# Kernel optimization log

Hardware: AMD Instinct MI355X
Metric: run time of the kernel (lower is better)

Reference implementation:

```python
import jax, jax.numpy as jnp
import numpy as np

EPS = 1e-5
T = 8          # n_segment
PATCH = 3      # corr_size


def _bn(x, g, b):
    # eval-mode BatchNorm with running_mean=0, running_var=1 (init values)
    shape = (1, -1) + (1,) * (x.ndim - 2)
    inv = 1.0 / jnp.sqrt(1.0 + EPS)
    return x * (g * inv).reshape(shape) + b.reshape(shape)


def setup_inputs() -> dict:
    key = jax.random.key(0)
    k1, k2, k3 = jax.random.split(key, 3)
    nt, c, h, w = 64, 256, 56, 56
    cr = 64  # c // reduction, reduction = 4
    return {
        "x": jax.random.normal(k1, (nt, c, h, w), dtype=jnp.float32),
        "conv21_w": jax.random.normal(k2, (cr, c), dtype=jnp.float32) * 0.05,
        "bn21_g": jnp.ones((cr,), jnp.float32),
        "bn21_b": jnp.zeros((cr,), jnp.float32),
        "bn22_g": jnp.ones((PATCH * PATCH,), jnp.float32),
        "bn22_b": jnp.zeros((PATCH * PATCH,), jnp.float32),
        "conv22_w": jax.random.normal(k3, (c, PATCH * PATCH), dtype=jnp.float32) * 0.05,
        "bn23_g": jnp.ones((c,), jnp.float32),
        "bn23_b": jnp.zeros((c,), jnp.float32),
    }


def reference(x, conv21_w, bn21_g, bn21_b, bn22_g, bn22_b, conv22_w, bn23_g, bn23_b):
    nt, c, h, w = x.shape
    n = nt // T
    cr = conv21_w.shape[0]
    residual = x

    # (n, c, T, h, w)
    xv = x.reshape(n, T, c, h, w).transpose(0, 2, 1, 3, 4)
    # conv21: 1x1x1 Conv3d c -> cr, no bias
    y = jnp.einsum('oc,ncthw->nothw', conv21_w, xv)
    y = jax.nn.relu(_bn(y, bn21_g, bn21_b))

    # temporally shifted copy: frame t paired with frame min(t+1, T-1)
    idx = jnp.minimum(jnp.arange(1, T + 1), T - 1)
    y2 = y[:, :, idx, :, :]

    # flatten back to (nt, cr, h, w)
    x1 = y.transpose(0, 2, 1, 3, 4).reshape(nt, cr, h, w)
    x2 = y2.transpose(0, 2, 1, 3, 4).reshape(nt, cr, h, w)

    # SpatialCorrelationSampler(kernel_size=1, patch_size=3): zero-padded
    # displacements (dy, dx) in {-1,0,1}^2, dot product over channels.
    pad = PATCH // 2
    x2p = jnp.pad(x2, ((0, 0), (0, 0), (pad, pad), (pad, pad)))
    cv = jnp.stack(
        [jnp.einsum('nchw,nchw->nhw', x1, x2p[:, :, dy:dy + h, dx:dx + w])
         for dy in range(PATCH) for dx in range(PATCH)],
        axis=1,
    ) / cr  # (nt, 9, h, w), divided by c // (reduction * corr_group)

    cv = jax.nn.relu(_bn(cv, bn22_g, bn22_b))
    # conv22: 1x1 Conv2d 9 -> c, no bias
    out = jnp.einsum('ok,nkhw->nohw', conv22_w, cv)
    out = _bn(out, bn23_g, bn23_b) + residual
    return jax.nn.relu(out)
```

## Files before the change

kernel.cpp:

```cpp
#include <hip/hip_runtime.h>

#define HW     3136
#define WIDTH  56
#define C      256
#define CR     64
#define NT     64
#define TT     8
#define PW     64
#define PH     58
#define YPLANE (PH*PW)
#define YBYTES ((size_t)NT * CR * YPLANE * 2)
#define CVBYTES ((size_t)NT * 9 * HW * 4)

#define BN_INV 0.9999950000374997f

typedef __attribute__((ext_vector_type(8))) short short8;
typedef __attribute__((ext_vector_type(8))) unsigned short ushort8;
typedef __attribute__((ext_vector_type(4))) float f32x4;
typedef __attribute__((ext_vector_type(2))) float f32x2;

static __device__ __forceinline__ float relu(float v) { return fmaxf(v, 0.0f); }
static __device__ __forceinline__ float bf2f(unsigned short u) {
    return __builtin_bit_cast(float, (unsigned)u << 16);
}
static __device__ __forceinline__ unsigned short f2bf(float f) {
    unsigned u = __builtin_bit_cast(unsigned, f);
    unsigned r = (u + 0x7FFFu + ((u >> 16) & 1u)) >> 16;
    return (unsigned short)r;
}
static __device__ __forceinline__ unsigned pack2(float a, float b) {
    return (unsigned)f2bf(a) | ((unsigned)f2bf(b) << 16);
}

__global__ __launch_bounds__(256) void k0_cvt_w(const float* __restrict__ w,
                                                unsigned short* __restrict__ wbf) {
    int i = blockIdx.x * 256 + threadIdx.x;
    wbf[i] = f2bf(w[i]);
}

static __device__ __forceinline__ void halo_zero(int nt, int tid,
                                                 unsigned short* __restrict__ y) {
    const int ch = tid >> 2, part = tid & 3;
    unsigned short* pl = y + ((size_t)nt * CR + ch) * YPLANE;
    if (part == 0) {
        ushort8 z = (ushort8)0;
#pragma unroll
        for (int j = 0; j < 8; ++j) *(ushort8*)(pl + j * 8) = z;
    } else if (part == 1) {
        ushort8 z = (ushort8)0;
        unsigned short* q = pl + 57 * PW;
#pragma unroll
        for (int j = 0; j < 8; ++j) *(ushort8*)(q + j * 8) = z;
    } else if (part == 2) {
        for (int r = 1; r <= 28; ++r) {
            unsigned short* q = pl + r * PW + 57;
#pragma unroll
            for (int j = 0; j < 8; ++j) q[j] = 0;
        }
    } else {
        for (int r = 29; r <= 56; ++r) {
            unsigned short* q = pl + r * PW + 57;
#pragma unroll
            for (int j = 0; j < 8; ++j) q[j] = 0;
        }
        pl[PW] = 0;
    }
}

template<int TP>
__global__ __launch_bounds__(256) void k1_mfma(const float* __restrict__ x,
                                               const unsigned short* __restrict__ wbf,
                                               const float* __restrict__ g,
                                               const float* __restrict__ bb,
                                               unsigned short* __restrict__ y) {
    constexpr int NB = TP / 64;
    constexpr int NQ = TP / 4;
    __shared__ unsigned short Bl[2][NQ][136];

    const int tid  = threadIdx.x;
    const int lane = tid & 63;
    const int wv   = tid >> 6;

    int nt, px0;
    if (TP == 256) {
        if (blockIdx.x >= 768) { halo_zero(blockIdx.x - 768, tid, y); return; }
        nt = blockIdx.x / 12; px0 = (blockIdx.x % 12) * 256;
    } else {
        nt = blockIdx.x; px0 = 3072;
    }

    const int p4 = tid & (NQ - 1);
    const int c8 = tid / NQ;
    const bool active = (TP == 256) ? true : (c8 < 4);

    const float* xbase = x + (size_t)nt * (C * HW) + px0 + 4 * p4;
    const int frow = lane & 15;
    const int hi   = lane >> 4;
    const unsigned short* abase = wbf + frow * C + hi * 8;

    f32x4 acc[NB][4];
#pragma unroll
    for (int nb = 0; nb < NB; ++nb)
#pragma unroll
        for (int mb = 0; mb < 4; ++mb) acc[nb][mb] = (f32x4)0.0f;

    f32x4  xq[8];
    short8 afr[2][4];

#define LOADB(KS)                                                          \
    if (active) {                                                          \
        const float* _p = xbase + (size_t)((KS) * 32 + c8 * 8) * HW;       \
        _Pragma("unroll")                                                  \
        for (int j = 0; j < 8; ++j) xq[j] = *(const f32x4*)(_p + (size_t)j * HW); \
    }

#define LOADA(KS, DST)                                                     \
    _Pragma("unroll")                                                      \
    for (int mb = 0; mb < 4; ++mb)                                         \
        (DST)[mb] = *(const short8*)(abase + mb * 16 * C + (KS) * 32);

#define WRITEB(BUF)                                                        \
    if (active) {                                                          \
        _Pragma("unroll")                                                  \
        for (int i = 0; i < 4; ++i) {                                      \
            union { unsigned d[4]; short8 v; } pk;                         \
            pk.d[0] = pack2(xq[0][i], xq[1][i]);                           \
            pk.d[1] = pack2(xq[2][i], xq[3][i]);                           \
            pk.d[2] = pack2(xq[4][i], xq[5][i]);                           \
            pk.d[3] = pack2(xq[6][i], xq[7][i]);                           \
            *(short8*)&Bl[BUF][p4][i * 32 + ((c8 ^ i) & 3) * 8] = pk.v;    \
        }                                                                  \
    }

    LOADB(0)
    LOADA(0, afr[0])
    WRITEB(0)
    __syncthreads();

#pragma unroll
    for (int ks = 0; ks < 8; ++ks) {
        const int cb = ks & 1;
        if (ks < 7) {
            LOADB(ks + 1)
            LOADA(ks + 1, afr[cb ^ 1])
        }
        short8 bfrag[NB];
#pragma unroll
        for (int nb = 0; nb < NB; ++nb) {
            const int pxl = wv * (TP / 4) + nb * 16 + frow;
            bfrag[nb] = *(const short8*)
                &Bl[cb][pxl >> 2][(pxl & 3) * 32 + ((hi ^ (pxl & 3)) & 3) * 8];
        }
#pragma unroll
        for (int nb = 0; nb < NB; ++nb)
#pragma unroll
            for (int mb = 0; mb < 4; ++mb)
                acc[nb][mb] = __builtin_amdgcn_mfma_f32_16x16x32_bf16(
                    afr[cb][mb], bfrag[nb], acc[nb][mb], 0, 0, 0);
        if (ks < 7) {
            WRITEB(cb ^ 1)
            __syncthreads();
        }
    }
#undef LOADB
#undef LOADA
#undef WRITEB

    unsigned short* ybase = y + (size_t)nt * CR * YPLANE;
#pragma unroll
    for (int nb = 0; nb < NB; ++nb) {
        const int p = px0 + wv * (TP / 4) + nb * 16 + frow;
        const int r = p / WIDTH;
        const int c = p - r * WIDTH;
        const int pidx = (r + 1) * PW + (c + 1);
#pragma unroll
        for (int mb = 0; mb < 4; ++mb)
#pragma unroll
            for (int rr = 0; rr < 4; ++rr) {
                int o = mb * 16 + hi * 4 + rr;
                float v = relu(fmaf(acc[nb][mb][rr], g[o] * BN_INV, bb[o]));
                ybase[(size_t)o * YPLANE + pidx] = f2bf(v);
            }
    }
}

__global__ __launch_bounds__(256) void k2_corr(const unsigned short* __restrict__ y,
                                               const float* __restrict__ g,
                                               const float* __restrict__ bb,
                                               float* __restrict__ cv) {
    int gt   = blockIdx.x * 256 + threadIdx.x;
    int h    = gt & 3;
    int task = gt >> 2;
    int nt   = task / 392;
    int rm   = task - nt * 392;
    int r    = rm / 7;
    int cg   = rm - r * 7;
    int c0   = cg * 8;
    int nt2  = ((nt & (TT - 1)) < TT - 1) ? nt + 1 : nt;

    const unsigned short* y1 = y + ((size_t)nt * CR + h * 16) * YPLANE
                                 + (size_t)(r + 1) * PW + c0;
    const unsigned short* y2 = y + ((size_t)nt2 * CR + h * 16) * YPLANE
                                 + (size_t)r * PW + c0;

    float acc[9][8];
#pragma unroll
    for (int k = 0; k < 9; ++k)
#pragma unroll
        for (int px = 0; px < 8; ++px) acc[k][px] = 0.0f;

#pragma unroll 2
    for (int ch = 0; ch < 16; ++ch) {
        const unsigned short* p1 = y1 + (size_t)ch * YPLANE;
        ushort8 a8 = *(const ushort8*)p1;
        unsigned at = *(const unsigned*)(p1 + 8);
        float a[8];
#pragma unroll
        for (int j = 0; j < 7; ++j) a[j] = bf2f(a8[j + 1]);
        a[7] = bf2f((unsigned short)(at & 0xffffu));

        const unsigned short* p2 = y2 + (size_t)ch * YPLANE;
#pragma unroll
        for (int dy = 0; dy < 3; ++dy) {
            const unsigned short* pr = p2 + dy * PW;
            ushort8 b8 = *(const ushort8*)pr;
            unsigned bt = *(const unsigned*)(pr + 8);
            float w[10];
#pragma unroll
            for (int j = 0; j < 8; ++j) w[j] = bf2f(b8[j]);
            w[8] = bf2f((unsigned short)(bt & 0xffffu));
            w[9] = bf2f((unsigned short)(bt >> 16));
#pragma unroll
            for (int dx = 0; dx < 3; ++dx) {
                int k = dy * 3 + dx;
#pragma unroll
                for (int px = 0; px < 8; ++px)
                    acc[k][px] = fmaf(a[px], w[px + dx], acc[k][px]);
            }
        }
    }

#pragma unroll
    for (int k = 0; k < 9; ++k)
#pragma unroll
        for (int px = 0; px < 8; ++px) {
            float v = acc[k][px];
            v += __shfl_xor(v, 1);
            v += __shfl_xor(v, 2);
            acc[k][px] = v;
        }

    if (h == 0) {
        float* cp = cv + (size_t)nt * 9 * HW + r * WIDTH + c0;
        const float rcr = 1.0f / CR;
#pragma unroll
        for (int k = 0; k < 9; ++k) {
            float sc = g[k] * BN_INV, bv = bb[k];
            f32x4 lo, hi;
            lo.x = relu(fmaf(acc[k][0] * rcr, sc, bv));
            lo.y = relu(fmaf(acc[k][1] * rcr, sc, bv));
            lo.z = relu(fmaf(acc[k][2] * rcr, sc, bv));
            lo.w = relu(fmaf(acc[k][3] * rcr, sc, bv));
            hi.x = relu(fmaf(acc[k][4] * rcr, sc, bv));
            hi.y = relu(fmaf(acc[k][5] * rcr, sc, bv));
            hi.z = relu(fmaf(acc[k][6] * rcr, sc, bv));
            hi.w = relu(fmaf(acc[k][7] * rcr, sc, bv));
            *(f32x4*)(cp + (size_t)k * HW)     = lo;
            *(f32x4*)(cp + (size_t)k * HW + 4) = hi;
        }
    }
}

__global__ __launch_bounds__(256) void k3_conv22(const float* __restrict__ cv,
                                                 const float* __restrict__ w2,
                                                 const float* __restrict__ g,
                                                 const float* __restrict__ bb,
                                                 const float* __restrict__ x,
                                                 float* __restrict__ out) {
    int gt = blockIdx.x * 256 + threadIdx.x;
    int nt = gt / 1568;
    int p2 = (gt - nt * 1568) * 2;

    const float* cp = cv + (size_t)nt * 9 * HW + p2;
    float cvx[9], cvy[9];
#pragma unroll
    for (int k = 0; k < 9; ++k) {
        f32x2 v = *(const f32x2*)(cp + (size_t)k * HW);
        cvx[k] = v.x; cvy[k] = v.y;
    }

    const float* xp = x   + (size_t)nt * (C * HW) + p2;
    float*       op = out + (size_t)nt * (C * HW) + p2;

#pragma unroll 8
    for (int o = 0; o < C; ++o) {
        const float* wr = w2 + o * 9;
        f32x2 xr = *(const f32x2*)(xp + (size_t)o * HW);
        float sx = 0.0f, sy = 0.0f;
#pragma unroll
        for (int k = 0; k < 9; ++k) {
            float wv = wr[k];
            sx = fmaf(wv, cvx[k], sx);
            sy = fmaf(wv, cvy[k], sy);
        }
        float sc = g[o] * BN_INV, bv = bb[o];
        f32x2 rv;
        rv.x = relu(fmaf(sx, sc, bv) + xr.x);
        rv.y = relu(fmaf(sy, sc, bv) + xr.y);
        *(f32x2*)(op + (size_t)o * HW) = rv;
    }
}

extern "C" void kernel_launch(void* const* d_in, const int* in_sizes, int n_in,
                              void* d_out, int out_size, void* d_ws, size_t ws_size,
                              hipStream_t stream) {
    const float* x   = (const float*)d_in[0];
    const float* w21 = (const float*)d_in[1];
    const float* g21 = (const float*)d_in[2];
    const float* b21 = (const float*)d_in[3];
    const float* g22 = (const float*)d_in[4];
    const float* b22 = (const float*)d_in[5];
    const float* w22 = (const float*)d_in[6];
    const float* g23 = (const float*)d_in[7];
    const float* b23 = (const float*)d_in[8];
    float* out = (float*)d_out;

    unsigned short* yb  = (unsigned short*)d_ws;
    float*          cvb = (float*)((char*)d_ws + YBYTES);
    unsigned short* wbf = (unsigned short*)((char*)d_ws + YBYTES + CVBYTES);

    k0_cvt_w     <<<64,  256, 0, stream>>>(w21, wbf);
    k1_mfma<256> <<<832, 256, 0, stream>>>(x, wbf, g21, b21, yb);
    k1_mfma<64>  <<<64,  256, 0, stream>>>(x, wbf, g21, b21, yb);
    k2_corr      <<<392, 256, 0, stream>>>(yb, g22, b22, cvb);
    k3_conv22    <<<392, 256, 0, stream>>>(cvb, w22, g23, b23, x, out);
}
```

Baseline: 195.7 us.

## Shrink per-thread work across all stages to raise block counts and occupancy

Measured after the change: 202.3 us. 3.3% more time.

```diff
diff --git a/kernel.cpp b/kernel.cpp
--- a/kernel.cpp
+++ b/kernel.cpp
@@ -23,6 +23,12 @@
 static __device__ __forceinline__ float bf2f(unsigned short u) {
     return __builtin_bit_cast(float, (unsigned)u << 16);
 }
+static __device__ __forceinline__ float bfLO(unsigned u) {
+    return __builtin_bit_cast(float, u << 16);
+}
+static __device__ __forceinline__ float bfHI(unsigned u) {
+    return __builtin_bit_cast(float, u & 0xFFFF0000u);
+}
 static __device__ __forceinline__ unsigned short f2bf(float f) {
     unsigned u = __builtin_bit_cast(unsigned, f);
     unsigned r = (u + 0x7FFFu + ((u >> 16) & 1u)) >> 16;
@@ -82,16 +88,16 @@
     const int wv   = tid >> 6;
 
     int nt, px0;
-    if (TP == 256) {
-        if (blockIdx.x >= 768) { halo_zero(blockIdx.x - 768, tid, y); return; }
-        nt = blockIdx.x / 12; px0 = (blockIdx.x % 12) * 256;
+    if (TP == 128) {
+        if (blockIdx.x >= 1536) { halo_zero(blockIdx.x - 1536, tid, y); return; }
+        nt = blockIdx.x / 24; px0 = (blockIdx.x % 24) * 128;
     } else {
         nt = blockIdx.x; px0 = 3072;
     }
 
     const int p4 = tid & (NQ - 1);
     const int c8 = tid / NQ;
-    const bool active = (TP == 256) ? true : (c8 < 4);
+    const bool active = (c8 < 4);
 
     const float* xbase = x + (size_t)nt * (C * HW) + px0 + 4 * p4;
     const int frow = lane & 15;
@@ -105,7 +111,7 @@
         for (int mb = 0; mb < 4; ++mb) acc[nb][mb] = (f32x4)0.0f;
 
     f32x4  xq[8];
-    short8 afr[2][4];
+    short8 afr[4];
 
 #define LOADB(KS)                                                          \
     if (active) {                                                          \
@@ -113,11 +119,6 @@
         _Pragma("unroll")                                                  \
         for (int j = 0; j < 8; ++j) xq[j] = *(const f32x4*)(_p + (size_t)j * HW); \
     }
-
-#define LOADA(KS, DST)                                                     \
-    _Pragma("unroll")                                                      \
-    for (int mb = 0; mb < 4; ++mb)                                         \
-        (DST)[mb] = *(const short8*)(abase + mb * 16 * C + (KS) * 32);
 
 #define WRITEB(BUF)                                                        \
     if (active) {                                                          \
@@ -133,17 +134,16 @@
     }
 
     LOADB(0)
-    LOADA(0, afr[0])
     WRITEB(0)
     __syncthreads();
 
 #pragma unroll
     for (int ks = 0; ks < 8; ++ks) {
         const int cb = ks & 1;
-        if (ks < 7) {
-            LOADB(ks + 1)
-            LOADA(ks + 1, afr[cb ^ 1])
-        }
+        if (ks < 7) { LOADB(ks + 1) }
+#pragma unroll
+        for (int mb = 0; mb < 4; ++mb)
+            afr[mb] = *(const short8*)(abase + mb * 16 * C + ks * 32);
         short8 bfrag[NB];
 #pragma unroll
         for (int nb = 0; nb < NB; ++nb) {
@@ -156,14 +156,13 @@
 #pragma unroll
             for (int mb = 0; mb < 4; ++mb)
                 acc[nb][mb] = __builtin_amdgcn_mfma_f32_16x16x32_bf16(
-                    afr[cb][mb], bfrag[nb], acc[nb][mb], 0, 0, 0);
+                    afr[mb], bfrag[nb], acc[nb][mb], 0, 0, 0);
         if (ks < 7) {
             WRITEB(cb ^ 1)
             __syncthreads();
         }
     }
 #undef LOADB
-#undef LOADA
 #undef WRITEB
 
     unsigned short* ybase = y + (size_t)nt * CR * YPLANE;
@@ -188,53 +187,44 @@
                                                const float* __restrict__ g,
                                                const float* __restrict__ bb,
                                                float* __restrict__ cv) {
-    int gt   = blockIdx.x * 256 + threadIdx.x;
-    int h    = gt & 3;
-    int task = gt >> 2;
-    int nt   = task / 392;
-    int rm   = task - nt * 392;
-    int r    = rm / 7;
-    int cg   = rm - r * 7;
-    int c0   = cg * 8;
-    int nt2  = ((nt & (TT - 1)) < TT - 1) ? nt + 1 : nt;
-
-    const unsigned short* y1 = y + ((size_t)nt * CR + h * 16) * YPLANE
-                                 + (size_t)(r + 1) * PW + c0;
-    const unsigned short* y2 = y + ((size_t)nt2 * CR + h * 16) * YPLANE
-                                 + (size_t)r * PW + c0;
-
-    float acc[9][8];
+    const int gt   = blockIdx.x * 256 + threadIdx.x;
+    const int h    = gt & 7;
+    const int task = gt >> 3;
+    const int nt   = task / 784;
+    const int rm   = task - nt * 784;
+    const int r    = rm / 14;
+    const int cg   = rm - r * 14;
+    const int c0   = cg * 4;
+    const int nt2  = ((nt & (TT - 1)) < TT - 1) ? nt + 1 : nt;
+
+    const unsigned* y1 = (const unsigned*)(y + ((size_t)nt * CR + h * 8) * YPLANE
+                                             + (size_t)(r + 1) * PW + c0);
+    const unsigned* y2 = (const unsigned*)(y + ((size_t)nt2 * CR + h * 8) * YPLANE
+                                             + (size_t)r * PW + c0);
+
+    float acc[9][4];
 #pragma unroll
     for (int k = 0; k < 9; ++k)
 #pragma unroll
-        for (int px = 0; px < 8; ++px) acc[k][px] = 0.0f;
-
-#pragma unroll 2
-    for (int ch = 0; ch < 16; ++ch) {
-        const unsigned short* p1 = y1 + (size_t)ch * YPLANE;
-        ushort8 a8 = *(const ushort8*)p1;
-        unsigned at = *(const unsigned*)(p1 + 8);
-        float a[8];
-#pragma unroll
-        for (int j = 0; j < 7; ++j) a[j] = bf2f(a8[j + 1]);
-        a[7] = bf2f((unsigned short)(at & 0xffffu));
-
-        const unsigned short* p2 = y2 + (size_t)ch * YPLANE;
+        for (int px = 0; px < 4; ++px) acc[k][px] = 0.0f;
+
+#pragma unroll
+    for (int ch = 0; ch < 8; ++ch) {
+        const unsigned* p1 = y1 + ch * (YPLANE / 2);
+        unsigned u0 = p1[0], u1 = p1[1], u2 = p1[2];
+        float a[4] = { bfHI(u0), bfLO(u1), bfHI(u1), bfLO(u2) };
+
+        const unsigned* p2 = y2 + ch * (YPLANE / 2);
 #pragma unroll
         for (int dy = 0; dy < 3; ++dy) {
-            const unsigned short* pr = p2 + dy * PW;
-            ushort8 b8 = *(const ushort8*)pr;
-            unsigned bt = *(const unsigned*)(pr + 8);
-            float w[10];
-#pragma unroll
-            for (int j = 0; j < 8; ++j) w[j] = bf2f(b8[j]);
-            w[8] = bf2f((unsigned short)(bt & 0xffffu));
-            w[9] = bf2f((unsigned short)(bt >> 16));
+            const unsigned* pr = p2 + dy * (PW / 2);
+            unsigned v0 = pr[0], v1 = pr[1], v2 = pr[2];
+            float w[6] = { bfLO(v0), bfHI(v0), bfLO(v1), bfHI(v1), bfLO(v2), bfHI(v2) };
 #pragma unroll
             for (int dx = 0; dx < 3; ++dx) {
                 int k = dy * 3 + dx;
 #pragma unroll
-                for (int px = 0; px < 8; ++px)
+                for (int px = 0; px < 4; ++px)
                     acc[k][px] = fmaf(a[px], w[px + dx], acc[k][px]);
             }
         }
@@ -243,10 +233,11 @@
 #pragma unroll
     for (int k = 0; k < 9; ++k)
 #pragma unroll
-        for (int px = 0; px < 8; ++px) {
+        for (int px = 0; px < 4; ++px) {
             float v = acc[k][px];
             v += __shfl_xor(v, 1);
             v += __shfl_xor(v, 2);
+            v += __shfl_xor(v, 4);
             acc[k][px] = v;
         }
 
@@ -256,17 +247,12 @@
 #pragma unroll
         for (int k = 0; k < 9; ++k) {
             float sc = g[k] * BN_INV, bv = bb[k];
-            f32x4 lo, hi;
-            lo.x = relu(fmaf(acc[k][0] * rcr, sc, bv));
-            lo.y = relu(fmaf(acc[k][1] * rcr, sc, bv));
-            lo.z = relu(fmaf(acc[k][2] * rcr, sc, bv));
-            lo.w = relu(fmaf(acc[k][3] * rcr, sc, bv));
-            hi.x = relu(fmaf(acc[k][4] * rcr, sc, bv));
-            hi.y = relu(fmaf(acc[k][5] * rcr, sc, bv));
-            hi.z = relu(fmaf(acc[k][6] * rcr, sc, bv));
-            hi.w = relu(fmaf(acc[k][7] * rcr, sc, bv));
-            *(f32x4*)(cp + (size_t)k * HW)     = lo;
-            *(f32x4*)(cp + (size_t)k * HW + 4) = hi;
+            f32x4 o;
+            o.x = relu(fmaf(acc[k][0] * rcr, sc, bv));
+            o.y = relu(fmaf(acc[k][1] * rcr, sc, bv));
+            o.z = relu(fmaf(acc[k][2] * rcr, sc, bv));
+            o.w = relu(fmaf(acc[k][3] * rcr, sc, bv));
+            *(f32x4*)(cp + (size_t)k * HW) = o;
         }
     }
 }
@@ -277,37 +263,30 @@
                                                  const float* __restrict__ bb,
                                                  const float* __restrict__ x,
                                                  float* __restrict__ out) {
-    int gt = blockIdx.x * 256 + threadIdx.x;
-    int nt = gt / 1568;
-    int p2 = (gt - nt * 1568) * 2;
-
-    const float* cp = cv + (size_t)nt * 9 * HW + p2;
-    float cvx[9], cvy[9];
-#pragma unroll
-    for (int k = 0; k < 9; ++k) {
-        f32x2 v = *(const f32x2*)(cp + (size_t)k * HW);
-        cvx[k] = v.x; cvy[k] = v.y;
-    }
-
-    const float* xp = x   + (size_t)nt * (C * HW) + p2;
-    float*       op = out + (size_t)nt * (C * HW) + p2;
+    const int ht  = (blockIdx.x >= 784);
+    const int pxg = (blockIdx.x - ht * 784) * 256 + threadIdx.x;
+    const int nt  = pxg / HW;
+    const int p   = pxg - nt * HW;
+    const int ob  = ht * 128;
+
+    const float* cp = cv + (size_t)nt * 9 * HW + p;
+    float cvv[9];
+#pragma unroll
+    for (int k = 0; k < 9; ++k) cvv[k] = cp[(size_t)k * HW];
+
+    const float* xp = x   + (size_t)nt * (C * HW) + (size_t)ob * HW + p;
+    float*       op = out + (size_t)nt * (C * HW) + (size_t)ob * HW + p;
 
 #pragma unroll 8
-    for (int o = 0; o < C; ++o) {
+    for (int oi = 0; oi < 128; ++oi) {
+        const int o = ob + oi;
         const float* wr = w2 + o * 9;
-        f32x2 xr = *(const f32x2*)(xp + (size_t)o * HW);
-        float sx = 0.0f, sy = 0.0f;
-#pragma unroll
-        for (int k = 0; k < 9; ++k) {
-            float wv = wr[k];
-            sx = fmaf(wv, cvx[k], sx);
-            sy = fmaf(wv, cvy[k], sy);
-        }
-        float sc = g[o] * BN_INV, bv = bb[o];
-        f32x2 rv;
-        rv.x = relu(fmaf(sx, sc, bv) + xr.x);
-        rv.y = relu(fmaf(sy, sc, bv) + xr.y);
-        *(f32x2*)(op + (size_t)o * HW) = rv;
+        float xr = xp[(size_t)oi * HW];
+        float s = 0.0f;
+#pragma unroll
+        for (int k = 0; k < 9; ++k) s = fmaf(wr[k], cvv[k], s);
+        float v = fmaf(s, g[o] * BN_INV, bb[o]) + xr;
+        op[(size_t)oi * HW] = relu(v);
     }
 }
 
@@ -329,9 +308,9 @@
     float*          cvb = (float*)((char*)d_ws + YBYTES);
     unsigned short* wbf = (unsigned short*)((char*)d_ws + YBYTES + CVBYTES);
 
-    k0_cvt_w     <<<64,  256, 0, stream>>>(w21, wbf);
-    k1_mfma<256> <<<832, 256, 0, stream>>>(x, wbf, g21, b21, yb);
-    k1_mfma<64>  <<<64,  256, 0, stream>>>(x, wbf, g21, b21, yb);
-    k2_corr      <<<392, 256, 0, stream>>>(yb, g22, b22, cvb);
-    k3_conv22    <<<392, 256, 0, stream>>>(cvb, w22, g23, b23, x, out);
-}
+    k0_cvt_w     <<<64,   256, 0, stream>>>(w21, wbf);
+    k1_mfma<128> <<<1600, 256, 0, stream>>>(x, wbf, g21, b21, yb);
+    k1_mfma<64>  <<<64,   256, 0, stream>>>(x, wbf, g21, b21, yb);
+    k2_corr      <<<1568, 256, 0, stream>>>(yb, g22, b22, cvb);
+    k3_conv22    <<<1568, 256, 0, stream>>>(cvb, w22, g23, b23, x, out);
+}
```

## Retile conv21 MFMA kernel to 64-pixel blocks with deeper load pipeline

Applied to the files above, without the earlier changes.

New measurement: 201.4 us. 1.03x slower.

```diff
diff --git a/kernel.cpp b/kernel.cpp
--- a/kernel.cpp
+++ b/kernel.cpp
@@ -67,121 +67,99 @@
     }
 }
 
-template<int TP>
 __global__ __launch_bounds__(256) void k1_mfma(const float* __restrict__ x,
                                                const unsigned short* __restrict__ wbf,
                                                const float* __restrict__ g,
                                                const float* __restrict__ bb,
                                                unsigned short* __restrict__ y) {
-    constexpr int NB = TP / 64;
-    constexpr int NQ = TP / 4;
-    __shared__ unsigned short Bl[2][NQ][136];
-
-    const int tid  = threadIdx.x;
+    const int blk = blockIdx.x;
+    const int tid = threadIdx.x;
+    if (blk >= 3136) { halo_zero(blk - 3136, tid, y); return; }
+
+    __shared__ unsigned short Bl[2][64][40];
+
     const int lane = tid & 63;
     const int wv   = tid >> 6;
-
-    int nt, px0;
-    if (TP == 256) {
-        if (blockIdx.x >= 768) { halo_zero(blockIdx.x - 768, tid, y); return; }
-        nt = blockIdx.x / 12; px0 = (blockIdx.x % 12) * 256;
-    } else {
-        nt = blockIdx.x; px0 = 3072;
-    }
-
-    const int p4 = tid & (NQ - 1);
-    const int c8 = tid / NQ;
-    const bool active = (TP == 256) ? true : (c8 < 4);
-
-    const float* xbase = x + (size_t)nt * (C * HW) + px0 + 4 * p4;
+    const int nt   = blk / 49;
+    const int p0   = (blk - nt * 49) * 64;
     const int frow = lane & 15;
     const int hi   = lane >> 4;
-    const unsigned short* abase = wbf + frow * C + hi * 8;
-
-    f32x4 acc[NB][4];
-#pragma unroll
-    for (int nb = 0; nb < NB; ++nb)
-#pragma unroll
-        for (int mb = 0; mb < 4; ++mb) acc[nb][mb] = (f32x4)0.0f;
-
-    f32x4  xq[8];
+
+    const float* xp = x + (size_t)nt * (C * HW) + p0 + lane;
+    const unsigned short* ab = wbf + frow * C + hi * 8;
+
+    f32x4 acc[4];
+#pragma unroll
+    for (int mb = 0; mb < 4; ++mb) acc[mb] = (f32x4)0.0f;
+
+    float  xq[2][8];
     short8 afr[2][4];
 
-#define LOADB(KS)                                                          \
-    if (active) {                                                          \
-        const float* _p = xbase + (size_t)((KS) * 32 + c8 * 8) * HW;       \
-        _Pragma("unroll")                                                  \
-        for (int j = 0; j < 8; ++j) xq[j] = *(const f32x4*)(_p + (size_t)j * HW); \
-    }
-
-#define LOADA(KS, DST)                                                     \
-    _Pragma("unroll")                                                      \
-    for (int mb = 0; mb < 4; ++mb)                                         \
-        (DST)[mb] = *(const short8*)(abase + mb * 16 * C + (KS) * 32);
-
-#define WRITEB(BUF)                                                        \
-    if (active) {                                                          \
-        _Pragma("unroll")                                                  \
-        for (int i = 0; i < 4; ++i) {                                      \
-            union { unsigned d[4]; short8 v; } pk;                         \
-            pk.d[0] = pack2(xq[0][i], xq[1][i]);                           \
-            pk.d[1] = pack2(xq[2][i], xq[3][i]);                           \
-            pk.d[2] = pack2(xq[4][i], xq[5][i]);                           \
-            pk.d[3] = pack2(xq[6][i], xq[7][i]);                           \
-            *(short8*)&Bl[BUF][p4][i * 32 + ((c8 ^ i) & 3) * 8] = pk.v;    \
-        }                                                                  \
-    }
-
-    LOADB(0)
-    LOADA(0, afr[0])
-    WRITEB(0)
-    __syncthreads();
+#define ISSUE_X(KS, SLOT)                                                   \
+    _Pragma("unroll")                                                       \
+    for (int j = 0; j < 8; ++j)                                             \
+        xq[SLOT][j] = xp[(size_t)((KS) * 32 + wv * 8 + j) * HW];
+
+#define ISSUE_A(KS, SLOT)                                                   \
+    _Pragma("unroll")                                                       \
+    for (int mb = 0; mb < 4; ++mb)                                          \
+        afr[SLOT][mb] = *(const short8*)(ab + mb * 16 * C + (KS) * 32);
+
+#define PACK_WRITE(SLOT, BUF)                                               \
+    {                                                                       \
+        union { unsigned d[4]; short8 v; } pk;                              \
+        pk.d[0] = pack2(xq[SLOT][0], xq[SLOT][1]);                          \
+        pk.d[1] = pack2(xq[SLOT][2], xq[SLOT][3]);                          \
+        pk.d[2] = pack2(xq[SLOT][4], xq[SLOT][5]);                          \
+        pk.d[3] = pack2(xq[SLOT][6], xq[SLOT][7]);                          \
+        *(short8*)&Bl[BUF][lane][wv * 8] = pk.v;                            \
+    }
+
+#define LDS_BARRIER                                                         \
+    __builtin_amdgcn_sched_barrier(0);                                      \
+    asm volatile("s_waitcnt lgkmcnt(0)" ::: "memory");                      \
+    __builtin_amdgcn_s_barrier();                                           \
+    __builtin_amdgcn_sched_barrier(0);
+
+    ISSUE_X(0, 0)
+    ISSUE_A(0, 0)
+    PACK_WRITE(0, 0)
+    ISSUE_X(1, 1)
+    LDS_BARRIER
 
 #pragma unroll
     for (int ks = 0; ks < 8; ++ks) {
         const int cb = ks & 1;
+        if (ks < 6) { ISSUE_X(ks + 2, cb) }
+        if (ks < 7) { ISSUE_A(ks + 1, cb ^ 1) }
+        short8 bf = *(const short8*)&Bl[cb][wv * 16 + frow][hi * 8];
+#pragma unroll
+        for (int mb = 0; mb < 4; ++mb)
+            acc[mb] = __builtin_amdgcn_mfma_f32_16x16x32_bf16(
+                afr[cb][mb], bf, acc[mb], 0, 0, 0);
         if (ks < 7) {
-            LOADB(ks + 1)
-            LOADA(ks + 1, afr[cb ^ 1])
-        }
-        short8 bfrag[NB];
-#pragma unroll
-        for (int nb = 0; nb < NB; ++nb) {
-            const int pxl = wv * (TP / 4) + nb * 16 + frow;
-            bfrag[nb] = *(const short8*)
-                &Bl[cb][pxl >> 2][(pxl & 3) * 32 + ((hi ^ (pxl & 3)) & 3) * 8];
-        }
-#pragma unroll
-        for (int nb = 0; nb < NB; ++nb)
-#pragma unroll
-            for (int mb = 0; mb < 4; ++mb)
-                acc[nb][mb] = __builtin_amdgcn_mfma_f32_16x16x32_bf16(
-                    afr[cb][mb], bfrag[nb], acc[nb][mb], 0, 0, 0);
-        if (ks < 7) {
-            WRITEB(cb ^ 1)
-            __syncthreads();
-        }
-    }
-#undef LOADB
-#undef LOADA
-#undef WRITEB
+            PACK_WRITE(cb ^ 1, cb ^ 1)
+            LDS_BARRIER
+        }
+    }
+#undef ISSUE_X
+#undef ISSUE_A
+#undef PACK_WRITE
+#undef LDS_BARRIER
 
     unsigned short* ybase = y + (size_t)nt * CR * YPLANE;
-#pragma unroll
-    for (int nb = 0; nb < NB; ++nb) {
-        const int p = px0 + wv * (TP / 4) + nb * 16 + frow;
-        const int r = p / WIDTH;
-        const int c = p - r * WIDTH;
-        const int pidx = (r + 1) * PW + (c + 1);
-#pragma unroll
-        for (int mb = 0; mb < 4; ++mb)
-#pragma unroll
-            for (int rr = 0; rr < 4; ++rr) {
-                int o = mb * 16 + hi * 4 + rr;
-                float v = relu(fmaf(acc[nb][mb][rr], g[o] * BN_INV, bb[o]));
-                ybase[(size_t)o * YPLANE + pidx] = f2bf(v);
-            }
-    }
+    const int p = p0 + wv * 16 + frow;
+    const int r = p / WIDTH;
+    const int c = p - r * WIDTH;
+    const int pidx = (r + 1) * PW + (c + 1);
+#pragma unroll
+    for (int mb = 0; mb < 4; ++mb)
+#pragma unroll
+        for (int rr = 0; rr < 4; ++rr) {
+            int o = mb * 16 + hi * 4 + rr;
+            float v = relu(fmaf(acc[mb][rr], g[o] * BN_INV, bb[o]));
+            ybase[(size_t)o * YPLANE + pidx] = f2bf(v);
+        }
 }
 
 __global__ __launch_bounds__(256) void k2_corr(const unsigned short* __restrict__ y,
@@ -329,9 +307,8 @@
     float*          cvb = (float*)((char*)d_ws + YBYTES);
     unsigned short* wbf = (unsigned short*)((char*)d_ws + YBYTES + CVBYTES);
 
-    k0_cvt_w     <<<64,  256, 0, stream>>>(w21, wbf);
-    k1_mfma<256> <<<832, 256, 0, stream>>>(x, wbf, g21, b21, yb);
-    k1_mfma<64>  <<<64,  256, 0, stream>>>(x, wbf, g21, b21, yb);
-    k2_corr      <<<392, 256, 0, stream>>>(yb, g22, b22, cvb);
-    k3_conv22    <<<392, 256, 0, stream>>>(cvb, w22, g23, b23, x, out);
-}
+    k0_cvt_w <<<64,   256, 0, stream>>>(w21, wbf);
+    k1_mfma  <<<3200, 256, 0, stream>>>(x, wbf, g21, b21, yb);
+    k2_corr  <<<392,  256, 0, stream>>>(yb, g22, b22, cvb);
+    k3_conv22<<<392,  256, 0, stream>>>(cvb, w22, g23, b23, x, out);
+}
```

## Restructure conv21 MFMA kernel with 384-pixel tiles and channel-major LDS staging

Applied to the files above, without the earlier changes.

Measured after the change: 191.8 us. 1.02x faster.

```diff
diff --git a/kernel.cpp b/kernel.cpp
--- a/kernel.cpp
+++ b/kernel.cpp
@@ -15,6 +15,7 @@
 #define BN_INV 0.9999950000374997f
 
 typedef __attribute__((ext_vector_type(8))) short short8;
+typedef __attribute__((ext_vector_type(4))) short s16x4;
 typedef __attribute__((ext_vector_type(8))) unsigned short ushort8;
 typedef __attribute__((ext_vector_type(4))) float f32x4;
 typedef __attribute__((ext_vector_type(2))) float f32x2;
@@ -67,109 +68,102 @@
     }
 }
 
-template<int TP>
+template<int NPX>
 __global__ __launch_bounds__(256) void k1_mfma(const float* __restrict__ x,
                                                const unsigned short* __restrict__ wbf,
                                                const float* __restrict__ g,
                                                const float* __restrict__ bb,
                                                unsigned short* __restrict__ y) {
-    constexpr int NB = TP / 64;
-    constexpr int NQ = TP / 4;
-    __shared__ unsigned short Bl[2][NQ][136];
+    constexpr int NFR = NPX / 64;
+    constexpr int NF4 = NPX / 32;
+    constexpr int NPW = NPX / 4;
+    constexpr int RS  = (NPX == 384) ? 394 : 66;
+    __shared__ unsigned short Bl[32][RS];
 
     const int tid  = threadIdx.x;
     const int lane = tid & 63;
     const int wv   = tid >> 6;
+    const int frow = lane & 15;
+    const int hi   = lane >> 4;
 
     int nt, px0;
-    if (TP == 256) {
-        if (blockIdx.x >= 768) { halo_zero(blockIdx.x - 768, tid, y); return; }
-        nt = blockIdx.x / 12; px0 = (blockIdx.x % 12) * 256;
+    if (NPX == 384) {
+        if (blockIdx.x >= 512) { halo_zero(blockIdx.x - 512, tid, y); return; }
+        nt = blockIdx.x >> 3; px0 = (blockIdx.x & 7) * 384;
     } else {
         nt = blockIdx.x; px0 = 3072;
     }
 
-    const int p4 = tid & (NQ - 1);
-    const int c8 = tid / NQ;
-    const bool active = (TP == 256) ? true : (c8 < 4);
-
-    const float* xbase = x + (size_t)nt * (C * HW) + px0 + 4 * p4;
-    const int frow = lane & 15;
-    const int hi   = lane >> 4;
-    const unsigned short* abase = wbf + frow * C + hi * 8;
-
-    f32x4 acc[NB][4];
-#pragma unroll
-    for (int nb = 0; nb < NB; ++nb)
+    const float* xbase = x + (size_t)nt * (C * HW) + px0;
+    const unsigned short* ab = wbf + frow * C + hi * 8;
+
+    int goff[NF4];
+    int doff[NF4];
+#pragma unroll
+    for (int j = 0; j < NF4; ++j) {
+        int f  = j * 256 + tid;
+        int c  = f / (NPX / 4);
+        int p4 = f - c * (NPX / 4);
+        goff[j] = c * HW + p4 * 4;
+        doff[j] = (c * RS + p4 * 4) * 2;
+    }
+
+    f32x4 acc[NFR][4];
+#pragma unroll
+    for (int nb = 0; nb < NFR; ++nb)
 #pragma unroll
         for (int mb = 0; mb < 4; ++mb) acc[nb][mb] = (f32x4)0.0f;
 
-    f32x4  xq[8];
-    short8 afr[2][4];
-
-#define LOADB(KS)                                                          \
-    if (active) {                                                          \
-        const float* _p = xbase + (size_t)((KS) * 32 + c8 * 8) * HW;       \
-        _Pragma("unroll")                                                  \
-        for (int j = 0; j < 8; ++j) xq[j] = *(const f32x4*)(_p + (size_t)j * HW); \
-    }
-
-#define LOADA(KS, DST)                                                     \
-    _Pragma("unroll")                                                      \
-    for (int mb = 0; mb < 4; ++mb)                                         \
-        (DST)[mb] = *(const short8*)(abase + mb * 16 * C + (KS) * 32);
-
-#define WRITEB(BUF)                                                        \
-    if (active) {                                                          \
-        _Pragma("unroll")                                                  \
-        for (int i = 0; i < 4; ++i) {                                      \
-            union { unsigned d[4]; short8 v; } pk;                         \
-            pk.d[0] = pack2(xq[0][i], xq[1][i]);                           \
-            pk.d[1] = pack2(xq[2][i], xq[3][i]);                           \
-            pk.d[2] = pack2(xq[4][i], xq[5][i]);                           \
-            pk.d[3] = pack2(xq[6][i], xq[7][i]);                           \
-            *(short8*)&Bl[BUF][p4][i * 32 + ((c8 ^ i) & 3) * 8] = pk.v;    \
-        }                                                                  \
-    }
-
-    LOADB(0)
-    LOADA(0, afr[0])
-    WRITEB(0)
-    __syncthreads();
+    f32x4 xq[NF4];
+
+#define ISSUE(KS)                                                           \
+    _Pragma("unroll")                                                       \
+    for (int j = 0; j < NF4; ++j)                                           \
+        xq[j] = *(const f32x4*)(xbase + (size_t)(KS) * (32 * HW) + goff[j]);
+
+#define PACKW                                                               \
+    _Pragma("unroll")                                                       \
+    for (int j = 0; j < NF4; ++j) {                                         \
+        union { unsigned d[2]; s16x4 v; } pk;                               \
+        pk.d[0] = pack2(xq[j].x, xq[j].y);                                  \
+        pk.d[1] = pack2(xq[j].z, xq[j].w);                                  \
+        *(s16x4*)((char*)&Bl[0][0] + doff[j]) = pk.v;                       \
+    }
+
+    ISSUE(0)
 
 #pragma unroll
     for (int ks = 0; ks < 8; ++ks) {
-        const int cb = ks & 1;
-        if (ks < 7) {
-            LOADB(ks + 1)
-            LOADA(ks + 1, afr[cb ^ 1])
-        }
-        short8 bfrag[NB];
-#pragma unroll
-        for (int nb = 0; nb < NB; ++nb) {
-            const int pxl = wv * (TP / 4) + nb * 16 + frow;
-            bfrag[nb] = *(const short8*)
-                &Bl[cb][pxl >> 2][(pxl & 3) * 32 + ((hi ^ (pxl & 3)) & 3) * 8];
-        }
-#pragma unroll
-        for (int nb = 0; nb < NB; ++nb)
+        __syncthreads();
+        PACKW
+        if (ks < 7) { ISSUE(ks + 1) }
+        __syncthreads();
+
+        short8 afr[4];
+#pragma unroll
+        for (int mb = 0; mb < 4; ++mb)
+            afr[mb] = *(const short8*)(ab + mb * 16 * C + ks * 32);
+
+#pragma unroll
+        for (int nb = 0; nb < NFR; ++nb) {
+            const int px = wv * NPW + nb * 16 + frow;
+            short8 bf;
+#pragma unroll
+            for (int j = 0; j < 8; ++j)
+                bf[j] = (short)Bl[hi * 8 + j][px];
 #pragma unroll
             for (int mb = 0; mb < 4; ++mb)
                 acc[nb][mb] = __builtin_amdgcn_mfma_f32_16x16x32_bf16(
-                    afr[cb][mb], bfrag[nb], acc[nb][mb], 0, 0, 0);
-        if (ks < 7) {
-            WRITEB(cb ^ 1)
-            __syncthreads();
-        }
-    }
-#undef LOADB
-#undef LOADA
-#undef WRITEB
+                    afr[mb], bf, acc[nb][mb], 0, 0, 0);
+        }
+    }
+#undef ISSUE
+#undef PACKW
 
     unsigned short* ybase = y + (size_t)nt * CR * YPLANE;
 #pragma unroll
-    for (int nb = 0; nb < NB; ++nb) {
-        const int p = px0 + wv * (TP / 4) + nb * 16 + frow;
+    for (int nb = 0; nb < NFR; ++nb) {
+        const int p = px0 + wv * NPW + nb * 16 + frow;
         const int r = p / WIDTH;
         const int c = p - r * WIDTH;
         const int pidx = (r + 1) * PW + (c + 1);
@@ -329,9 +323,9 @@
     float*          cvb = (float*)((char*)d_ws + YBYTES);
     unsigned short* wbf = (unsigned short*)((char*)d_ws + YBYTES + CVBYTES);
 
-    k0_cvt_w     <<<64,  256, 0, stream>>>(w21, wbf);
-    k1_mfma<256> <<<832, 256, 0, stream>>>(x, wbf, g21, b21, yb);
-    k1_mfma<64>  <<<64,  256, 0, stream>>>(x, wbf, g21, b21, yb);
-    k2_corr      <<<392, 256, 0, stream>>>(yb, g22, b22, cvb);
-    k3_conv22    <<<392, 256, 0, stream>>>(cvb, w22, g23, b23, x, out);
-}
+    k0_cvt_w    <<<64,  256, 0, stream>>>(w21, wbf);
+    k1_mfma<384><<<576, 256, 0, stream>>>(x, wbf, g21, b21, yb);
+    k1_mfma<64> <<<64,  256, 0, stream>>>(x, wbf, g21, b21, yb);
+    k2_corr     <<<392, 256, 0, stream>>>(yb, g22, b22, cvb);
+    k3_conv22   <<<392, 256, 0, stream>>>(cvb, w22, g23, b23, x, out);
+}
```
